# Kernel tuning notes

Hardware: AMD Instinct MI355X
Metric: run time of the kernel (lower is better)

The kernel has to match this reference:

```python
import jax, jax.numpy as jnp
import numpy as np

MARGIN = 0.3


def setup_inputs() -> dict:
    key = jax.random.key(0)
    k1, k2 = jax.random.split(key)
    embeddings = jax.random.normal(k1, (4096, 128), dtype=jnp.float32)
    labels = jax.random.randint(k2, (4096,), 0, 256, dtype=jnp.int64)
    return {"embeddings": embeddings, "labels": labels}


def reference(embeddings, labels):
    # L2-normalize rows (same as F.normalize(p=2, dim=1), eps=1e-12)
    norm = jnp.maximum(jnp.linalg.norm(embeddings, axis=1, keepdims=True), 1e-12)
    e = embeddings / norm
    # cosine distance matrix [N, N]
    dist = 1.0 - e @ e.T

    same = labels[None, :] == labels[:, None]          # [N, N]
    n = labels.shape[0]
    eye = jnp.eye(n, dtype=bool)
    pos_mask = same & ~eye                             # positives excl. self
    neg_mask = ~same

    # dist in [0, 2]; finite sentinels keep max/min well-defined per row
    hardest_pos = jnp.max(jnp.where(pos_mask, dist, -1.0), axis=1)
    hardest_neg = jnp.min(jnp.where(neg_mask, dist, 3.0), axis=1)

    valid = jnp.any(pos_mask, axis=1) & jnp.any(neg_mask, axis=1)
    per_row = jax.nn.relu(hardest_pos - hardest_neg + MARGIN)
    loss_sum = jnp.sum(jnp.where(valid, per_row, 0.0))
    count = jnp.sum(valid)
    return loss_sum / jnp.maximum(count, 1).astype(loss_sum.dtype)
```

## Files before the change

kernel.cpp:

```cpp
#include <hip/hip_runtime.h>
#include <stdint.h>

typedef __bf16 bf16x8 __attribute__((ext_vector_type(8)));
typedef float f32x4 __attribute__((ext_vector_type(4)));

#define N_ROWS 4096
#define KD 128
#define BM 64
#define BN 64
#define LDA 136
#define NCHUNK 16
#define CHUNK 256

__device__ __forceinline__ unsigned short f32_to_bf16_rne(float f) {
    union { float f; uint32_t u; } v; v.f = f;
    uint32_t u = v.u;
    return (unsigned short)((u + 0x7FFFu + ((u >> 16) & 1u)) >> 16);
}

__global__ __launch_bounds__(256) void normalize_kernel(const float* __restrict__ E,
                                                        unsigned short* __restrict__ out) {
    const int wave = threadIdx.x >> 6;
    const int lane = threadIdx.x & 63;
    const int row = blockIdx.x * 4 + wave;
    const float2 v = *(const float2*)&E[row * KD + lane * 2];
    float s = v.x * v.x + v.y * v.y;
#pragma unroll
    for (int m = 1; m < 64; m <<= 1) s += __shfl_xor(s, m, 64);
    float inv = 0.0f;
    if (s > 0.0f) {
        inv = rsqrtf(s);
        inv = inv * (1.5f - 0.5f * s * inv * inv);
    }
    const unsigned short a = f32_to_bf16_rne(v.x * inv);
    const unsigned short b = f32_to_bf16_rne(v.y * inv);
    ((uint32_t*)out)[row * (KD / 2) + lane] = ((uint32_t)b << 16) | a;
}

__global__ __launch_bounds__(256) void gram_kernel(const unsigned short* __restrict__ Ebits,
                                                   const int* __restrict__ labels,
                                                   float* __restrict__ minpos_part,
                                                   float* __restrict__ maxneg_part) {
    __shared__ unsigned short As[BM * LDA];
    __shared__ unsigned short Bs[BN * LDA];
    __shared__ int ljs[CHUNK];

    const int tid = threadIdx.x;
    const int itile = blockIdx.x & 63;
    const int chunk = blockIdx.x >> 6;
    const int ibase = itile * BM;
    const int cbase = chunk * CHUNK;

    {
        const uint4* src = (const uint4*)(Ebits + (size_t)ibase * KD);
#pragma unroll
        for (int it = 0; it < 4; ++it) {
            const int li = tid + it * 256;
            const int r = li >> 4, c = li & 15;
            *(uint4*)&As[r * LDA + c * 8] = src[li];
        }
        ljs[tid] = labels[cbase + tid];
    }
    __syncthreads();

    const int wave = tid >> 6, lane = tid & 63;
    const int quad = lane >> 4, l15 = lane & 15;

    bf16x8 afrag[4];
    const unsigned short* arow = &As[(wave * 16 + l15) * LDA + quad * 8];
#pragma unroll
    for (int s = 0; s < 4; ++s) afrag[s] = *(const bf16x8*)(arow + s * 32);

    int li_lab[4];
#pragma unroll
    for (int r = 0; r < 4; ++r) li_lab[r] = labels[ibase + wave * 16 + quad * 4 + r];

    float minpos[4] = {2.0f, 2.0f, 2.0f, 2.0f};
    float maxneg[4] = {-2.0f, -2.0f, -2.0f, -2.0f};

    for (int jt = 0; jt < CHUNK / BN; ++jt) {
        const int jbase = cbase + jt * BN;
        __syncthreads();
        {
            const uint4* src = (const uint4*)(Ebits + (size_t)jbase * KD);
#pragma unroll
            for (int it = 0; it < 4; ++it) {
                const int li = tid + it * 256;
                const int r = li >> 4, c = li & 15;
                *(uint4*)&Bs[r * LDA + c * 8] = src[li];
            }
        }
        __syncthreads();

#pragma unroll
        for (int t = 0; t < 4; ++t) {
            const unsigned short* brow = &Bs[(t * 16 + l15) * LDA + quad * 8];
            f32x4 acc = {0.f, 0.f, 0.f, 0.f};
#pragma unroll
            for (int s = 0; s < 4; ++s) {
                const bf16x8 bfrag = *(const bf16x8*)(brow + s * 32);
                acc = __builtin_amdgcn_mfma_f32_16x16x32_bf16(afrag[s], bfrag, acc, 0, 0, 0);
            }
            const int jg = jbase + t * 16 + l15;
            const int lj = ljs[jt * BN + t * 16 + l15];
#pragma unroll
            for (int r = 0; r < 4; ++r) {
                const int ig = ibase + wave * 16 + quad * 4 + r;
                const float d = acc[r];
                const bool same = (lj == li_lab[r]);
                const float dp = (same && (ig != jg)) ? d : 2.0f;
                const float dn = same ? -2.0f : d;
                minpos[r] = fminf(minpos[r], dp);
                maxneg[r] = fmaxf(maxneg[r], dn);
            }
        }
    }

#pragma unroll
    for (int m = 1; m < 16; m <<= 1) {
#pragma unroll
        for (int r = 0; r < 4; ++r) {
            minpos[r] = fminf(minpos[r], __shfl_xor(minpos[r], m, 64));
            maxneg[r] = fmaxf(maxneg[r], __shfl_xor(maxneg[r], m, 64));
        }
    }
    if (l15 == 0) {
#pragma unroll
        for (int r = 0; r < 4; ++r) {
            const int row = ibase + wave * 16 + quad * 4 + r;
            minpos_part[row * NCHUNK + chunk] = minpos[r];
            maxneg_part[row * NCHUNK + chunk] = maxneg[r];
        }
    }
}

__global__ __launch_bounds__(256) void finalize_kernel(const float* __restrict__ minpos_part,
                                                       const float* __restrict__ maxneg_part,
                                                       float* __restrict__ out) {
    __shared__ float ssum[4];
    __shared__ int scnt[4];
    float sum = 0.f;
    int cnt = 0;
    for (int row = threadIdx.x; row < N_ROWS; row += 256) {
        float mp = 2.f, mn = -2.f;
#pragma unroll
        for (int c4 = 0; c4 < NCHUNK / 4; ++c4) {
            const float4 p = ((const float4*)minpos_part)[row * (NCHUNK / 4) + c4];
            const float4 q = ((const float4*)maxneg_part)[row * (NCHUNK / 4) + c4];
            mp = fminf(mp, fminf(fminf(p.x, p.y), fminf(p.z, p.w)));
            mn = fmaxf(mn, fmaxf(fmaxf(q.x, q.y), fmaxf(q.z, q.w)));
        }
        if (mp < 1.5f && mn > -1.5f) {
            sum += fmaxf(0.f, mn - mp + 0.3f);
            cnt += 1;
        }
    }
#pragma unroll
    for (int m = 1; m < 64; m <<= 1) {
        sum += __shfl_xor(sum, m, 64);
        cnt += __shfl_xor(cnt, m, 64);
    }
    const int wave = threadIdx.x >> 6, lane = threadIdx.x & 63;
    if (lane == 0) { ssum[wave] = sum; scnt[wave] = cnt; }
    __syncthreads();
    if (threadIdx.x == 0) {
        const float S = ssum[0] + ssum[1] + ssum[2] + ssum[3];
        const int C = scnt[0] + scnt[1] + scnt[2] + scnt[3];
        out[0] = S / (float)(C > 0 ? C : 1);
    }
}

extern "C" void kernel_launch(void* const* d_in, const int* in_sizes, int n_in,
                              void* d_out, int out_size, void* d_ws, size_t ws_size,
                              hipStream_t stream) {
    const float* E = (const float*)d_in[0];
    const int* labels = (const int*)d_in[1];

    unsigned short* ebits = (unsigned short*)d_ws;
    float* minpos_part = (float*)((char*)d_ws + (size_t)N_ROWS * KD * 2);
    float* maxneg_part = minpos_part + N_ROWS * NCHUNK;
    float* out = (float*)d_out;

    normalize_kernel<<<N_ROWS / 4, 256, 0, stream>>>(E, ebits);
    gram_kernel<<<64 * NCHUNK, 256, 0, stream>>>(ebits, labels, minpos_part, maxneg_part);
    finalize_kernel<<<1, 256, 0, stream>>>(minpos_part, maxneg_part, out);
}
```

Measured before the change: 78.34 us.

## Stage whole B chunk once via registers into swizzled LDS, read A directly

```diff
diff --git a/kernel.cpp b/kernel.cpp
--- a/kernel.cpp
+++ b/kernel.cpp
@@ -7,16 +7,18 @@
 #define N_ROWS 4096
 #define KD 128
 #define BM 64
-#define BN 64
-#define LDA 136
 #define NCHUNK 16
 #define CHUNK 256
+#define NBLOCKS (64 * NCHUNK)
 
 __device__ __forceinline__ unsigned short f32_to_bf16_rne(float f) {
     union { float f; uint32_t u; } v; v.f = f;
     uint32_t u = v.u;
     return (unsigned short)((u + 0x7FFFu + ((u >> 16) & 1u)) >> 16);
 }
+
+__device__ __forceinline__ int swz(int row, int c) { return row * 16 + (c ^ (row & 15)); }
+__device__ __forceinline__ int swzL(int L) { return (L & ~15) | ((L & 15) ^ ((L >> 4) & 15)); }
 
 __global__ __launch_bounds__(256) void normalize_kernel(const float* __restrict__ E,
                                                         unsigned short* __restrict__ out) {
@@ -37,12 +39,10 @@
     ((uint32_t*)out)[row * (KD / 2) + lane] = ((uint32_t)b << 16) | a;
 }
 
-__global__ __launch_bounds__(256) void gram_kernel(const unsigned short* __restrict__ Ebits,
-                                                   const int* __restrict__ labels,
-                                                   float* __restrict__ minpos_part,
-                                                   float* __restrict__ maxneg_part) {
-    __shared__ unsigned short As[BM * LDA];
-    __shared__ unsigned short Bs[BN * LDA];
+__global__ __launch_bounds__(256, 2) void gram_kernel(const unsigned short* __restrict__ Ebits,
+                                                      const int* __restrict__ labels,
+                                                      float2* __restrict__ partials) {
+    __shared__ uint4 Bs4[CHUNK * (KD / 8)];
     __shared__ int ljs[CHUNK];
 
     const int tid = threadIdx.x;
@@ -51,68 +51,54 @@
     const int ibase = itile * BM;
     const int cbase = chunk * CHUNK;
 
-    {
-        const uint4* src = (const uint4*)(Ebits + (size_t)ibase * KD);
-#pragma unroll
-        for (int it = 0; it < 4; ++it) {
-            const int li = tid + it * 256;
-            const int r = li >> 4, c = li & 15;
-            *(uint4*)&As[r * LDA + c * 8] = src[li];
-        }
-        ljs[tid] = labels[cbase + tid];
-    }
-    __syncthreads();
-
     const int wave = tid >> 6, lane = tid & 63;
     const int quad = lane >> 4, l15 = lane & 15;
+    const int igb = ibase + wave * 16 + quad * 4;
+
+    uint4 breg[16];
+    {
+        const uint4* bsrc = (const uint4*)(Ebits + (size_t)cbase * KD);
+#pragma unroll
+        for (int it = 0; it < 16; ++it) breg[it] = bsrc[it * 256 + tid];
+    }
+    ljs[tid] = labels[cbase + tid];
 
     bf16x8 afrag[4];
-    const unsigned short* arow = &As[(wave * 16 + l15) * LDA + quad * 8];
+    {
+        const uint4* asrc = (const uint4*)Ebits;
+        const int arow = ibase + wave * 16 + l15;
 #pragma unroll
-    for (int s = 0; s < 4; ++s) afrag[s] = *(const bf16x8*)(arow + s * 32);
-
+        for (int s = 0; s < 4; ++s) afrag[s] = *(const bf16x8*)&asrc[arow * 16 + s * 4 + quad];
+    }
     int li_lab[4];
 #pragma unroll
-    for (int r = 0; r < 4; ++r) li_lab[r] = labels[ibase + wave * 16 + quad * 4 + r];
+    for (int r = 0; r < 4; ++r) li_lab[r] = labels[igb + r];
+
+#pragma unroll
+    for (int it = 0; it < 16; ++it) Bs4[swzL(it * 256 + tid)] = breg[it];
+    __syncthreads();
 
     float minpos[4] = {2.0f, 2.0f, 2.0f, 2.0f};
     float maxneg[4] = {-2.0f, -2.0f, -2.0f, -2.0f};
 
-    for (int jt = 0; jt < CHUNK / BN; ++jt) {
-        const int jbase = cbase + jt * BN;
-        __syncthreads();
-        {
-            const uint4* src = (const uint4*)(Ebits + (size_t)jbase * KD);
+#pragma unroll 4
+    for (int t = 0; t < 16; ++t) {
+        f32x4 acc = {0.f, 0.f, 0.f, 0.f};
 #pragma unroll
-            for (int it = 0; it < 4; ++it) {
-                const int li = tid + it * 256;
-                const int r = li >> 4, c = li & 15;
-                *(uint4*)&Bs[r * LDA + c * 8] = src[li];
-            }
+        for (int s = 0; s < 4; ++s) {
+            const bf16x8 bfrag = *(const bf16x8*)&Bs4[swz(t * 16 + l15, s * 4 + quad)];
+            acc = __builtin_amdgcn_mfma_f32_16x16x32_bf16(afrag[s], bfrag, acc, 0, 0, 0);
         }
-        __syncthreads();
-
+        const int jg = cbase + t * 16 + l15;
+        const int lj = ljs[t * 16 + l15];
 #pragma unroll
-        for (int t = 0; t < 4; ++t) {
-            const unsigned short* brow = &Bs[(t * 16 + l15) * LDA + quad * 8];
-            f32x4 acc = {0.f, 0.f, 0.f, 0.f};
-#pragma unroll
-            for (int s = 0; s < 4; ++s) {
-                const bf16x8 bfrag = *(const bf16x8*)(brow + s * 32);
-                acc = __builtin_amdgcn_mfma_f32_16x16x32_bf16(afrag[s], bfrag, acc, 0, 0, 0);
-            }
-            const int jg = jbase + t * 16 + l15;
-            const int lj = ljs[jt * BN + t * 16 + l15];
-#pragma unroll
-            for (int r = 0; r < 4; ++r) {
-                const int ig = ibase + wave * 16 + quad * 4 + r;
-                const float d = acc[r];
-                const bool same = (lj == li_lab[r]);
-                const float dp = (same && (ig != jg)) ? d : 2.0f;
-                const float dn = same ? -2.0f : d;
-                minpos[r] = fminf(minpos[r], dp);
-                maxneg[r] = fmaxf(maxneg[r], dn);
-            }
+        for (int r = 0; r < 4; ++r) {
+            const float d = acc[r];
+            const bool same = (lj == li_lab[r]);
+            const float dp = (same && (igb + r != jg)) ? d : 2.0f;
+            const float dn = same ? -2.0f : d;
+            minpos[r] = fminf(minpos[r], dp);
+            maxneg[r] = fmaxf(maxneg[r], dn);
         }
     }
 
@@ -126,16 +112,12 @@
     }
     if (l15 == 0) {
 #pragma unroll
-        for (int r = 0; r < 4; ++r) {
-            const int row = ibase + wave * 16 + quad * 4 + r;
-            minpos_part[row * NCHUNK + chunk] = minpos[r];
-            maxneg_part[row * NCHUNK + chunk] = maxneg[r];
-        }
+        for (int r = 0; r < 4; ++r)
+            partials[(igb + r) * NCHUNK + chunk] = make_float2(minpos[r], maxneg[r]);
     }
 }
 
-__global__ __launch_bounds__(256) void finalize_kernel(const float* __restrict__ minpos_part,
-                                                       const float* __restrict__ maxneg_part,
+__global__ __launch_bounds__(256) void finalize_kernel(const float2* __restrict__ partials,
                                                        float* __restrict__ out) {
     __shared__ float ssum[4];
     __shared__ int scnt[4];
@@ -143,12 +125,12 @@
     int cnt = 0;
     for (int row = threadIdx.x; row < N_ROWS; row += 256) {
         float mp = 2.f, mn = -2.f;
+        const float4* p4 = (const float4*)&partials[row * NCHUNK];
 #pragma unroll
-        for (int c4 = 0; c4 < NCHUNK / 4; ++c4) {
-            const float4 p = ((const float4*)minpos_part)[row * (NCHUNK / 4) + c4];
-            const float4 q = ((const float4*)maxneg_part)[row * (NCHUNK / 4) + c4];
-            mp = fminf(mp, fminf(fminf(p.x, p.y), fminf(p.z, p.w)));
-            mn = fmaxf(mn, fmaxf(fmaxf(q.x, q.y), fmaxf(q.z, q.w)));
+        for (int c = 0; c < NCHUNK / 2; ++c) {
+            const float4 v = p4[c];
+            mp = fminf(mp, fminf(v.x, v.z));
+            mn = fmaxf(mn, fmaxf(v.y, v.w));
         }
         if (mp < 1.5f && mn > -1.5f) {
             sum += fmaxf(0.f, mn - mp + 0.3f);
@@ -177,11 +159,10 @@
     const int* labels = (const int*)d_in[1];
 
     unsigned short* ebits = (unsigned short*)d_ws;
-    float* minpos_part = (float*)((char*)d_ws + (size_t)N_ROWS * KD * 2);
-    float* maxneg_part = minpos_part + N_ROWS * NCHUNK;
+    float2* partials = (float2*)((char*)d_ws + (size_t)N_ROWS * KD * 2);
     float* out = (float*)d_out;
 
     normalize_kernel<<<N_ROWS / 4, 256, 0, stream>>>(E, ebits);
-    gram_kernel<<<64 * NCHUNK, 256, 0, stream>>>(ebits, labels, minpos_part, maxneg_part);
-    finalize_kernel<<<1, 256, 0, stream>>>(minpos_part, maxneg_part, out);
+    gram_kernel<<<NBLOCKS, 256, 0, stream>>>(ebits, labels, partials);
+    finalize_kernel<<<1, 256, 0, stream>>>(partials, out);
 }
```

Result: slower. 83.51 us (+6.6%).
